# Optimization experiments

Hardware: AMD Instinct MI355X
Metric: run time of the kernel (lower is better)

The kernel has to match this reference:

```python
import jax, jax.numpy as jnp
import numpy as np

B, T, C, H = 16, 2048, 192, 64

def setup_inputs() -> dict:
    key = jax.random.key(0)
    k1, k2, k3, k4 = jax.random.split(key, 4)
    x = jax.random.normal(k1, (B, T, C), dtype=jnp.float32)
    Wq = jax.random.normal(k2, (C, H), dtype=jnp.float32) * (C ** -0.5)
    Wk = jax.random.normal(k3, (C, H), dtype=jnp.float32) * (C ** -0.5)
    Wv = jax.random.normal(k4, (C, H), dtype=jnp.float32) * (C ** -0.5)
    return {"x": x, "Wq": Wq, "Wk": Wk, "Wv": Wv}

def reference(x, Wq, Wk, Wv):
    # One head of causal self-attention (dropout in eval mode / identity).
    q = x @ Wq                       # [B, T, H]
    k = x @ Wk                       # [B, T, H]
    v = x @ Wv                       # [B, T, H]
    scale = q.shape[-1] ** -0.5
    wei = jnp.einsum('bth,bsh->bts', q, k) * scale   # [B, T, T]
    t = wei.shape[-1]
    causal = jnp.tril(jnp.ones((t, t), dtype=bool))  # tril mask
    wei = jnp.where(causal, wei, -jnp.inf)
    wei = jax.nn.softmax(wei, axis=-1)
    out = jnp.einsum('bts,bsh->bth', wei, v)         # [B, T, H]
    return out
```

## Files before the change

### kernel.cpp

```cpp
#include <hip/hip_runtime.h>

#define B 16
#define T 2048
#define C 192
#define H 64

typedef __bf16 bf16x8 __attribute__((ext_vector_type(8)));
typedef __bf16 bf16x4 __attribute__((ext_vector_type(4)));
typedef float  f32x4  __attribute__((ext_vector_type(4)));

#define MFMA(a, b, c) __builtin_amdgcn_mfma_f32_16x16x32_bf16(a, b, c, 0, 0, 0)

#define SM_BIAS 24.0f

__global__ __launch_bounds__(256) void wtrans_kernel(
    const float* __restrict__ Wq, const float* __restrict__ Wk,
    const float* __restrict__ Wv, __bf16* __restrict__ wt)
{
    const int idx = blockIdx.x * 256 + threadIdx.x;
    const int n = idx / C;
    const int k = idx - n * C;
    const float* W = (n < 64) ? Wq : (n < 128) ? Wk : Wv;
    const int nc = n & 63;
    wt[n * C + k] = (__bf16)W[k * H + nc];
}

__global__ __launch_bounds__(256) void qkv_mfma_kernel(
    const float* __restrict__ x, const __bf16* __restrict__ wt,
    __bf16* __restrict__ qb, __bf16* __restrict__ kb, __bf16* __restrict__ vt)
{
    __shared__ __bf16 Ws[2][192][40];
    __shared__ __bf16 tile[64][72];

    const int tid  = threadIdx.x;
    const int w    = tid >> 6;
    const int lid  = tid & 15;
    const int quad = (tid & 63) >> 4;
    const int m0   = blockIdx.x * 64 + w * 16;

    const float* xrow = x + (size_t)(m0 + lid) * C + quad * 8;
    float4 a0[6], a1[6];
    #pragma unroll
    for (int kc = 0; kc < 6; kc++) {
        a0[kc] = *(const float4*)(xrow + kc * 32);
        a1[kc] = *(const float4*)(xrow + kc * 32 + 4);
    }
    bf16x8 af[6];
    #pragma unroll
    for (int kc = 0; kc < 6; kc++) {
        af[kc][0] = (__bf16)a0[kc].x; af[kc][1] = (__bf16)a0[kc].y;
        af[kc][2] = (__bf16)a0[kc].z; af[kc][3] = (__bf16)a0[kc].w;
        af[kc][4] = (__bf16)a1[kc].x; af[kc][5] = (__bf16)a1[kc].y;
        af[kc][6] = (__bf16)a1[kc].z; af[kc][7] = (__bf16)a1[kc].w;
    }

    bf16x8 wpf[3];
    auto prefW = [&](int kc) {
        #pragma unroll
        for (int i = 0; i < 3; i++) {
            const int p = i * 256 + tid;
            wpf[i] = *(const bf16x8*)(wt + (p >> 2) * C + kc * 32 + (p & 3) * 8);
        }
    };

    f32x4 acc[12] = {};
    prefW(0);
    int cur = 0;
    for (int kc = 0; kc < 6; kc++) {
        #pragma unroll
        for (int i = 0; i < 3; i++) {
            const int p = i * 256 + tid;
            *(bf16x8*)&Ws[cur][p >> 2][(p & 3) * 8] = wpf[i];
        }
        __syncthreads();
        if (kc < 5) prefW(kc + 1);
        #pragma unroll
        for (int nt = 0; nt < 12; nt++) {
            const bf16x8 bfr = *(const bf16x8*)&Ws[cur][nt * 16 + lid][quad * 8];
            acc[nt] = MFMA(af[kc], bfr, acc[nt]);
        }
        cur ^= 1;
    }

    #pragma unroll
    for (int nt = 0; nt < 8; nt++) {
        const int n = nt * 16 + lid;
        __bf16* dst = (n < 64) ? qb : kb;
        const int col = n & 63;
        const float scale = (n < 64) ? 0.1803368801111204f : 1.0f;
        #pragma unroll
        for (int r = 0; r < 4; r++) {
            const int row = m0 + quad * 4 + r;
            dst[(size_t)row * H + col] = (__bf16)(acc[nt][r] * scale);
        }
    }

    #pragma unroll
    for (int nt = 8; nt < 12; nt++) {
        const int col = (nt - 8) * 16 + lid;
        #pragma unroll
        for (int r = 0; r < 4; r++)
            tile[w * 16 + quad * 4 + r][col] = (__bf16)(acc[nt][r]);
    }
    __syncthreads();

    const int bb = blockIdx.x >> 5;
    const int t0 = (blockIdx.x & 31) << 6;
    #pragma unroll
    for (int it = 0; it < 2; ++it) {
        const int h   = it * 32 + (tid >> 3);
        const int tl0 = (tid & 7) * 8;
        bf16x8 d;
        #pragma unroll
        for (int j = 0; j < 8; j++) d[j] = tile[tl0 + j][h];
        *(bf16x8*)(vt + ((size_t)(bb * H + h)) * T + t0 + tl0) = d;
    }
}

__global__ __launch_bounds__(256, 1) void attn_kernel(
    const __bf16* __restrict__ qb,
    const __bf16* __restrict__ kb,
    const __bf16* __restrict__ vt,
    float* __restrict__ out)
{
    __shared__ __bf16 Kb[4][64][72];
    __shared__ __bf16 Vb[4][64][72];

    const int tid  = threadIdx.x;
    const int w    = tid >> 6;
    const int lid  = tid & 15;
    const int quad = (tid & 63) >> 4;

    const int b   = blockIdx.x & 15;
    const int pr  = blockIdx.x >> 4;
    const int qtH = 31 - pr, qtL = pr;
    const int nchH = qtH + 1;
    const int ntot = 33;
    const int nsteps = 17;
    const size_t bbase = (size_t)b * T;

    const int qH = (qtH << 6) + w * 16;
    const int qL = (qtL << 6) + w * 16;

    const __bf16* qrH = qb + (bbase + qH + lid) * H + quad * 8;
    const bf16x8 qfH0 = *(const bf16x8*)(qrH);
    const bf16x8 qfH1 = *(const bf16x8*)(qrH + 32);
    const __bf16* qrL = qb + (bbase + qL + lid) * H + quad * 8;
    const bf16x8 qfL0 = *(const bf16x8*)(qrL);
    const bf16x8 qfL1 = *(const bf16x8*)(qrL + 32);

    const __bf16* kgb = kb + bbase * H;
    const __bf16* vgb = vt + (size_t)b * H * T;

    const int ra = tid >> 3, ca = (tid & 7) * 8;
    const int rb = ra + 32,  cb = ca;

    auto keyof = [&](int i) {
        if (i >= ntot) i = ntot - 1;
        return (i < nchH ? i : i - nchH) << 6;
    };

    bf16x8 kra[2], krb[2], vra[2], vrb[2];
    auto prefetch2 = [&](int s) {
        #pragma unroll
        for (int u = 0; u < 2; u++) {
            const int key0 = keyof(2 * s + u);
            kra[u] = *(const bf16x8*)(kgb + (size_t)(key0 + ra) * H + ca);
            krb[u] = *(const bf16x8*)(kgb + (size_t)(key0 + rb) * H + cb);
            vra[u] = *(const bf16x8*)(vgb + (size_t)ra * T + key0 + ca);
            vrb[u] = *(const bf16x8*)(vgb + (size_t)rb * T + key0 + cb);
        }
    };

    f32x4 O[4] = {};
    float lsum = 0.f;

    auto epilogue = [&](int qw0) {
        float ls = lsum;
        ls += __shfl_xor(ls, 16, 64);
        ls += __shfl_xor(ls, 32, 64);
        #pragma unroll
        for (int ht = 0; ht < 4; ht++)
            #pragma unroll
            for (int r = 0; r < 4; r++) {
                const float Lr = __shfl(ls, quad * 4 + r, 16);
                out[(bbase + qw0 + quad * 4 + r) * H + ht * 16 + lid] =
                    O[ht][r] / Lr;
            }
    };

    bf16x8 cq0 = qfH0, cq1 = qfH1;
    int cqw = qH;

    prefetch2(0);
    int cur = 0;
    for (int s = 0; s < nsteps; s++) {
        #pragma unroll
        for (int u = 0; u < 2; u++) {
            const int buf = 2 * cur + u;
            *(bf16x8*)&Kb[buf][ra][ca] = kra[u];
            *(bf16x8*)&Kb[buf][rb][cb] = krb[u];
            *(bf16x8*)&Vb[buf][ra][ca] = vra[u];
            *(bf16x8*)&Vb[buf][rb][cb] = vrb[u];
        }
        __syncthreads();
        if (s + 1 < nsteps) prefetch2(s + 1);

        #pragma unroll
        for (int u = 0; u < 2; u++) {
            const int i = 2 * s + u;
            if (i >= ntot) break;
            if (i == nchH) {
                epilogue(cqw);
                #pragma unroll
                for (int ht = 0; ht < 4; ht++) O[ht] = (f32x4){0.f,0.f,0.f,0.f};
                lsum = 0.f;
                cq0 = qfL0; cq1 = qfL1; cqw = qL;
            }
            const int key0 = keyof(i);
            const int buf  = 2 * cur + u;

            bf16x8 kf[8];
            #pragma unroll
            for (int j = 0; j < 4; j++) {
                kf[2*j]   = *(const bf16x8*)&Kb[buf][j * 16 + lid][quad * 8];
                kf[2*j+1] = *(const bf16x8*)&Kb[buf][j * 16 + lid][32 + quad * 8];
            }
            bf16x8 bv0[4], bv1[4];
            #pragma unroll
            for (int ht = 0; ht < 4; ht++) {
                const __bf16* vr = &Vb[buf][ht * 16 + lid][quad * 4];
                ((bf16x4*)&bv0[ht])[0] = *(const bf16x4*)(vr);
                ((bf16x4*)&bv0[ht])[1] = *(const bf16x4*)(vr + 16);
                ((bf16x4*)&bv1[ht])[0] = *(const bf16x4*)(vr + 32);
                ((bf16x4*)&bv1[ht])[1] = *(const bf16x4*)(vr + 48);
            }

            bf16x8 af0, af1;
            const bool boundary = (key0 + 63 > cqw);
            #pragma unroll
            for (int j = 0; j < 4; j++) {
                f32x4 sS = {-SM_BIAS, -SM_BIAS, -SM_BIAS, -SM_BIAS};
                sS = MFMA(kf[2*j], cq0, sS);
                sS = MFMA(kf[2*j+1], cq1, sS);
                if (boundary) {
                    #pragma unroll
                    for (int r = 0; r < 4; r++)
                        if (key0 + j * 16 + quad * 4 + r > cqw + lid)
                            sS[r] = -1e30f;
                }
                #pragma unroll
                for (int r = 0; r < 4; r++) {
                    const float p = __builtin_amdgcn_exp2f(sS[r]);
                    lsum += p;
                    if      (j == 0) af0[r]     = (__bf16)p;
                    else if (j == 1) af0[4 + r] = (__bf16)p;
                    else if (j == 2) af1[r]     = (__bf16)p;
                    else             af1[4 + r] = (__bf16)p;
                }
            }

            #pragma unroll
            for (int ht = 0; ht < 4; ht++) {
                O[ht] = MFMA(af0, bv0[ht], O[ht]);
                O[ht] = MFMA(af1, bv1[ht], O[ht]);
            }
        }
        cur ^= 1;
    }
    epilogue(cqw);
}

extern "C" void kernel_launch(void* const* d_in, const int* in_sizes, int n_in,
                              void* d_out, int out_size, void* d_ws, size_t ws_size,
                              hipStream_t stream)
{
    const float* x  = (const float*)d_in[0];
    const float* Wq = (const float*)d_in[1];
    const float* Wk = (const float*)d_in[2];
    const float* Wv = (const float*)d_in[3];

    const size_t BTH = (size_t)B * T * H;
    __bf16* qbuf = (__bf16*)d_ws;
    __bf16* kbuf = qbuf + BTH;
    __bf16* vtb  = kbuf + BTH;
    __bf16* wt   = vtb + BTH;
    float* outp = (float*)d_out;

    wtrans_kernel<<<(C * 3 * H) / 256, 256, 0, stream>>>(Wq, Wk, Wv, wt);
    qkv_mfma_kernel<<<B * T / 64, 256, 0, stream>>>(x, wt, qbuf, kbuf, vtb);
    attn_kernel<<<B * T / 128, 256, 0, stream>>>(qbuf, kbuf, vtb, outp);
}
```

Baseline: 114.6 us.

## Split attention key chunks across two wave groups with shared-memory reduction

The attention block grows from 256 to 512 threads: two groups of four waves each take alternate key chunks from the same double-buffered tile load, and each keeps separate accumulators for the heavy and light query tiles. At the end, group 1 writes its partial outputs and row sums to shared memory and group 0 adds them and normalises. This halves the serial chunk loop per wave and raises waves per CU, in exchange for an extra shared-memory reduction, more registers (two accumulator sets), and a padded V stride of 68 that may change bank conflicts.

```diff
diff --git a/kernel.cpp b/kernel.cpp
--- a/kernel.cpp
+++ b/kernel.cpp
@@ -117,17 +117,19 @@
     }
 }
 
-__global__ __launch_bounds__(256, 1) void attn_kernel(
+__global__ __launch_bounds__(512, 2) void attn_kernel(
     const __bf16* __restrict__ qb,
     const __bf16* __restrict__ kb,
     const __bf16* __restrict__ vt,
     float* __restrict__ out)
 {
-    __shared__ __bf16 Kb[4][64][72];
-    __shared__ __bf16 Vb[4][64][72];
+    __shared__ __bf16 Kb[2][2][64][72];
+    __shared__ __bf16 Vb[2][2][64][68];
 
     const int tid  = threadIdx.x;
-    const int w    = tid >> 6;
+    const int wv   = tid >> 6;
+    const int grp  = wv >> 2;
+    const int w    = wv & 3;
     const int lid  = tid & 15;
     const int quad = (tid & 63) >> 4;
 
@@ -136,7 +138,6 @@
     const int qtH = 31 - pr, qtL = pr;
     const int nchH = qtH + 1;
     const int ntot = 33;
-    const int nsteps = 17;
     const size_t bbase = (size_t)b * T;
 
     const int qH = (qtH << 6) + w * 16;
@@ -153,122 +154,132 @@
     const __bf16* vgb = vt + (size_t)b * H * T;
 
     const int ra = tid >> 3, ca = (tid & 7) * 8;
-    const int rb = ra + 32,  cb = ca;
 
     auto keyof = [&](int i) {
-        if (i >= ntot) i = ntot - 1;
+        if (i > ntot - 1) i = ntot - 1;
         return (i < nchH ? i : i - nchH) << 6;
     };
 
-    bf16x8 kra[2], krb[2], vra[2], vrb[2];
-    auto prefetch2 = [&](int s) {
-        #pragma unroll
-        for (int u = 0; u < 2; u++) {
-            const int key0 = keyof(2 * s + u);
-            kra[u] = *(const bf16x8*)(kgb + (size_t)(key0 + ra) * H + ca);
-            krb[u] = *(const bf16x8*)(kgb + (size_t)(key0 + rb) * H + cb);
-            vra[u] = *(const bf16x8*)(vgb + (size_t)ra * T + key0 + ca);
-            vrb[u] = *(const bf16x8*)(vgb + (size_t)rb * T + key0 + cb);
+    bf16x8 kr[2], vr2[2];
+    auto prefetch = [&](int s) {
+        #pragma unroll
+        for (int g = 0; g < 2; g++) {
+            const int key0 = keyof(2 * s + g);
+            kr[g]  = *(const bf16x8*)(kgb + (size_t)(key0 + ra) * H + ca);
+            vr2[g] = *(const bf16x8*)(vgb + (size_t)ra * T + key0 + ca);
         }
     };
 
-    f32x4 O[4] = {};
-    float lsum = 0.f;
-
-    auto epilogue = [&](int qw0) {
-        float ls = lsum;
-        ls += __shfl_xor(ls, 16, 64);
-        ls += __shfl_xor(ls, 32, 64);
+    f32x4 OH[4] = {}, OL[4] = {};
+    float lsH = 0.f, lsL = 0.f;
+
+    auto doChunk = [&](f32x4 (&O)[4], float& ls, bf16x8 cq0, bf16x8 cq1,
+                       int cqw, int key0, int cur) {
+        const __bf16 (*Kc)[72] = Kb[cur][grp];
+        const __bf16 (*Vc)[68] = Vb[cur][grp];
+        bf16x8 kf[8];
+        #pragma unroll
+        for (int j = 0; j < 4; j++) {
+            kf[2*j]   = *(const bf16x8*)&Kc[j * 16 + lid][quad * 8];
+            kf[2*j+1] = *(const bf16x8*)&Kc[j * 16 + lid][32 + quad * 8];
+        }
+        bf16x8 bv0[4], bv1[4];
+        #pragma unroll
+        for (int ht = 0; ht < 4; ht++) {
+            const __bf16* vr_ = &Vc[ht * 16 + lid][quad * 4];
+            ((bf16x4*)&bv0[ht])[0] = *(const bf16x4*)(vr_);
+            ((bf16x4*)&bv0[ht])[1] = *(const bf16x4*)(vr_ + 16);
+            ((bf16x4*)&bv1[ht])[0] = *(const bf16x4*)(vr_ + 32);
+            ((bf16x4*)&bv1[ht])[1] = *(const bf16x4*)(vr_ + 48);
+        }
+        bf16x8 af0, af1;
+        const bool boundary = (key0 + 63 > cqw);
+        #pragma unroll
+        for (int j = 0; j < 4; j++) {
+            f32x4 sS = {-SM_BIAS, -SM_BIAS, -SM_BIAS, -SM_BIAS};
+            sS = MFMA(kf[2*j], cq0, sS);
+            sS = MFMA(kf[2*j+1], cq1, sS);
+            if (boundary) {
+                #pragma unroll
+                for (int r = 0; r < 4; r++)
+                    if (key0 + j * 16 + quad * 4 + r > cqw + lid) sS[r] = -1e30f;
+            }
+            #pragma unroll
+            for (int r = 0; r < 4; r++) {
+                const float p = __builtin_amdgcn_exp2f(sS[r]);
+                ls += p;
+                if      (j == 0) af0[r]     = (__bf16)p;
+                else if (j == 1) af0[4 + r] = (__bf16)p;
+                else if (j == 2) af1[r]     = (__bf16)p;
+                else             af1[4 + r] = (__bf16)p;
+            }
+        }
+        #pragma unroll
+        for (int ht = 0; ht < 4; ht++) {
+            O[ht] = MFMA(af0, bv0[ht], O[ht]);
+            O[ht] = MFMA(af1, bv1[ht], O[ht]);
+        }
+    };
+
+    prefetch(0);
+    int cur = 0;
+    for (int s = 0; s < 17; s++) {
+        *(bf16x8*)&Kb[cur][0][ra][ca] = kr[0];
+        *(bf16x8*)&Kb[cur][1][ra][ca] = kr[1];
+        *(bf16x8*)&Vb[cur][0][ra][ca] = vr2[0];
+        *(bf16x8*)&Vb[cur][1][ra][ca] = vr2[1];
+        __syncthreads();
+        if (s + 1 < 17) prefetch(s + 1);
+
+        const int i = 2 * s + grp;
+        if (i < ntot) {
+            const bool heavy = (i < nchH);
+            const int key0 = (heavy ? i : i - nchH) << 6;
+            if (heavy) doChunk(OH, lsH, qfH0, qfH1, qH, key0, cur);
+            else       doChunk(OL, lsL, qfL0, qfL1, qL, key0, cur);
+        }
+        cur ^= 1;
+    }
+
+    __syncthreads();
+    float* sO = (float*)&Kb[0][0][0][0];
+    float* sL = (float*)&Vb[0][0][0][0];
+
+    float lh = lsH; lh += __shfl_xor(lh, 16, 64); lh += __shfl_xor(lh, 32, 64);
+    float ll = lsL; ll += __shfl_xor(ll, 16, 64); ll += __shfl_xor(ll, 32, 64);
+
+    if (grp == 1) {
         #pragma unroll
         for (int ht = 0; ht < 4; ht++)
             #pragma unroll
             for (int r = 0; r < 4; r++) {
-                const float Lr = __shfl(ls, quad * 4 + r, 16);
-                out[(bbase + qw0 + quad * 4 + r) * H + ht * 16 + lid] =
-                    O[ht][r] / Lr;
+                sO[((0 * 4 + w) * 16 + quad * 4 + r) * 64 + ht * 16 + lid] = OH[ht][r];
+                sO[((1 * 4 + w) * 16 + quad * 4 + r) * 64 + ht * 16 + lid] = OL[ht][r];
             }
-    };
-
-    bf16x8 cq0 = qfH0, cq1 = qfH1;
-    int cqw = qH;
-
-    prefetch2(0);
-    int cur = 0;
-    for (int s = 0; s < nsteps; s++) {
-        #pragma unroll
-        for (int u = 0; u < 2; u++) {
-            const int buf = 2 * cur + u;
-            *(bf16x8*)&Kb[buf][ra][ca] = kra[u];
-            *(bf16x8*)&Kb[buf][rb][cb] = krb[u];
-            *(bf16x8*)&Vb[buf][ra][ca] = vra[u];
-            *(bf16x8*)&Vb[buf][rb][cb] = vrb[u];
-        }
-        __syncthreads();
-        if (s + 1 < nsteps) prefetch2(s + 1);
-
-        #pragma unroll
-        for (int u = 0; u < 2; u++) {
-            const int i = 2 * s + u;
-            if (i >= ntot) break;
-            if (i == nchH) {
-                epilogue(cqw);
-                #pragma unroll
-                for (int ht = 0; ht < 4; ht++) O[ht] = (f32x4){0.f,0.f,0.f,0.f};
-                lsum = 0.f;
-                cq0 = qfL0; cq1 = qfL1; cqw = qL;
+        if ((tid & 63) < 16) {
+            sL[(0 * 4 + w) * 16 + lid] = lh;
+            sL[(1 * 4 + w) * 16 + lid] = ll;
+        }
+    }
+    __syncthreads();
+    if (grp == 0) {
+        lh += sL[(0 * 4 + w) * 16 + lid];
+        ll += sL[(1 * 4 + w) * 16 + lid];
+        #pragma unroll
+        for (int ht = 0; ht < 4; ht++)
+            #pragma unroll
+            for (int r = 0; r < 4; r++) {
+                const float LrH = __shfl(lh, quad * 4 + r, 16);
+                const float vH = OH[ht][r]
+                    + sO[((0 * 4 + w) * 16 + quad * 4 + r) * 64 + ht * 16 + lid];
+                out[(bbase + qH + quad * 4 + r) * H + ht * 16 + lid] = vH / LrH;
+
+                const float LrL = __shfl(ll, quad * 4 + r, 16);
+                const float vL = OL[ht][r]
+                    + sO[((1 * 4 + w) * 16 + quad * 4 + r) * 64 + ht * 16 + lid];
+                out[(bbase + qL + quad * 4 + r) * H + ht * 16 + lid] = vL / LrL;
             }
-            const int key0 = keyof(i);
-            const int buf  = 2 * cur + u;
-
-            bf16x8 kf[8];
-            #pragma unroll
-            for (int j = 0; j < 4; j++) {
-                kf[2*j]   = *(const bf16x8*)&Kb[buf][j * 16 + lid][quad * 8];
-                kf[2*j+1] = *(const bf16x8*)&Kb[buf][j * 16 + lid][32 + quad * 8];
-            }
-            bf16x8 bv0[4], bv1[4];
-            #pragma unroll
-            for (int ht = 0; ht < 4; ht++) {
-                const __bf16* vr = &Vb[buf][ht * 16 + lid][quad * 4];
-                ((bf16x4*)&bv0[ht])[0] = *(const bf16x4*)(vr);
-                ((bf16x4*)&bv0[ht])[1] = *(const bf16x4*)(vr + 16);
-                ((bf16x4*)&bv1[ht])[0] = *(const bf16x4*)(vr + 32);
-                ((bf16x4*)&bv1[ht])[1] = *(const bf16x4*)(vr + 48);
-            }
-
-            bf16x8 af0, af1;
-            const bool boundary = (key0 + 63 > cqw);
-            #pragma unroll
-            for (int j = 0; j < 4; j++) {
-                f32x4 sS = {-SM_BIAS, -SM_BIAS, -SM_BIAS, -SM_BIAS};
-                sS = MFMA(kf[2*j], cq0, sS);
-                sS = MFMA(kf[2*j+1], cq1, sS);
-                if (boundary) {
-                    #pragma unroll
-                    for (int r = 0; r < 4; r++)
-                        if (key0 + j * 16 + quad * 4 + r > cqw + lid)
-                            sS[r] = -1e30f;
-                }
-                #pragma unroll
-                for (int r = 0; r < 4; r++) {
-                    const float p = __builtin_amdgcn_exp2f(sS[r]);
-                    lsum += p;
-                    if      (j == 0) af0[r]     = (__bf16)p;
-                    else if (j == 1) af0[4 + r] = (__bf16)p;
-                    else if (j == 2) af1[r]     = (__bf16)p;
-                    else             af1[4 + r] = (__bf16)p;
-                }
-            }
-
-            #pragma unroll
-            for (int ht = 0; ht < 4; ht++) {
-                O[ht] = MFMA(af0, bv0[ht], O[ht]);
-                O[ht] = MFMA(af1, bv1[ht], O[ht]);
-            }
-        }
-        cur ^= 1;
-    }
-    epilogue(cqw);
+    }
 }
 
 extern "C" void kernel_launch(void* const* d_in, const int* in_sizes, int n_in,
@@ -289,5 +300,5 @@
 
     wtrans_kernel<<<(C * 3 * H) / 256, 256, 0, stream>>>(Wq, Wk, Wv, wt);
     qkv_mfma_kernel<<<B * T / 64, 256, 0, stream>>>(x, wt, qbuf, kbuf, vtb);
-    attn_kernel<<<B * T / 128, 256, 0, stream>>>(qbuf, kbuf, vtb, outp);
+    attn_kernel<<<B * T / 128, 512, 0, stream>>>(qbuf, kbuf, vtb, outp);
 }
```

Result: faster. 105.7 us (-7.8%).
